# Optimization experiments

Measured on AMD Instinct MI355X. Metric: run time of the kernel, lower is better.

## Reference

```python
import jax, jax.numpy as jnp
import numpy as np

NUM_ENTITIES = 100000
NUM_RELATIONS = 500
EMB_DIM = 256
B = 128
N_CAND = 10000


def setup_inputs() -> dict:
    key = jax.random.key(0)
    k1, k2, k3, k4, k5 = jax.random.split(key, 5)
    # xavier_uniform bound for an (N, D) embedding matrix: sqrt(6/(N+D))
    be = float(np.sqrt(6.0 / (NUM_ENTITIES + EMB_DIM)))
    br = float(np.sqrt(6.0 / (NUM_RELATIONS + EMB_DIM)))
    entity_emb = jax.random.uniform(k1, (NUM_ENTITIES, EMB_DIM), jnp.float32, -be, be)
    relation_emb = jax.random.uniform(k2, (NUM_RELATIONS, EMB_DIM), jnp.float32, -br, br)
    heads = jax.random.randint(k3, (B,), 0, NUM_ENTITIES)
    relations = jax.random.randint(k4, (B,), 0, NUM_RELATIONS)
    tails = jax.random.randint(k5, (N_CAND,), 0, NUM_ENTITIES)
    return {
        "entity_emb": entity_emb,
        "relation_emb": relation_emb,
        "heads": heads,
        "relations": relations,
        "tails": tails,
    }


def reference(entity_emb, relation_emb, heads, relations, tails):
    # score_mode='multi_tails', p=2, dropout=0 (eval)
    h = entity_emb[heads]          # [B, D]
    r = relation_emb[relations]    # [B, D]
    t = entity_emb[tails]          # [N_cand, D]
    left = h + r                   # [B, D]
    # elementwise broadcast L2 distance (donot_use_mm_for_euclid_dist)
    diff = left[:, None, :] - t[None, :, :]          # [B, N_cand, D]
    out = -jnp.sqrt(jnp.sum(diff * diff, axis=-1))   # [B, N_cand]
    return out
```

## Files before the change

### kernel.cpp

```cpp
#include <hip/hip_runtime.h>
#include <math.h>


#define NUM_HEADS 128
#define NCAND     10000
#define EDIM      256
#define BM        64
#define BN        64
#define BK        16

__global__ __launch_bounds__(256) void transe_score_kernel(
    const float* __restrict__ entity,
    const float* __restrict__ relation,
    const int*   __restrict__ heads,
    const int*   __restrict__ relations,
    const int*   __restrict__ tails,
    float*       __restrict__ out)
{
    __shared__ float As[BK][BM];
    __shared__ float Bs[BK][BN];

    const int tid = threadIdx.x;
    const int n0  = blockIdx.x * BN;
    const int m0  = blockIdx.y * BM;

    const int srow = tid & 63;
    const int skq  = tid >> 6;

    const int am = m0 + srow;
    const float* __restrict__ pah = entity   + (size_t)heads[am]     * EDIM;
    const float* __restrict__ par = relation + (size_t)relations[am] * EDIM;

    int bn = n0 + srow;
    if (bn > NCAND - 1) bn = NCAND - 1;
    const float* __restrict__ pb = entity + (size_t)tails[bn] * EDIM;

    const int tx = tid & 15;
    const int ty = tid >> 4;

    float acc[4][4] = {};

    for (int k0 = 0; k0 < EDIM; k0 += BK) {
        float4 vh = *reinterpret_cast<const float4*>(pah + k0 + skq * 4);
        float4 vr = *reinterpret_cast<const float4*>(par + k0 + skq * 4);
        As[skq * 4 + 0][srow] = vh.x + vr.x;
        As[skq * 4 + 1][srow] = vh.y + vr.y;
        As[skq * 4 + 2][srow] = vh.z + vr.z;
        As[skq * 4 + 3][srow] = vh.w + vr.w;
        float4 vb = *reinterpret_cast<const float4*>(pb + k0 + skq * 4);
        Bs[skq * 4 + 0][srow] = vb.x;
        Bs[skq * 4 + 1][srow] = vb.y;
        Bs[skq * 4 + 2][srow] = vb.z;
        Bs[skq * 4 + 3][srow] = vb.w;
        __syncthreads();

        #pragma unroll
        for (int kk = 0; kk < BK; ++kk) {
            float4 a4 = *reinterpret_cast<const float4*>(&As[kk][ty * 4]);
            float4 b4 = *reinterpret_cast<const float4*>(&Bs[kk][tx * 4]);
            float a[4] = {a4.x, a4.y, a4.z, a4.w};
            float b[4] = {b4.x, b4.y, b4.z, b4.w};
            #pragma unroll
            for (int i = 0; i < 4; ++i)
                #pragma unroll
                for (int j = 0; j < 4; ++j) {
                    float d = a[i] - b[j];
                    acc[i][j] = fmaf(d, d, acc[i][j]);
                }
        }
        __syncthreads();
    }

    const int n = n0 + tx * 4;
    if (n < NCAND) {
        #pragma unroll
        for (int i = 0; i < 4; ++i) {
            const int m = m0 + ty * 4 + i;
            float4 o;
            o.x = -sqrtf(acc[i][0]);
            o.y = -sqrtf(acc[i][1]);
            o.z = -sqrtf(acc[i][2]);
            o.w = -sqrtf(acc[i][3]);
            *reinterpret_cast<float4*>(out + (size_t)m * NCAND + n) = o;
        }
    }
}

extern "C" void kernel_launch(void* const* d_in, const int* in_sizes, int n_in,
                              void* d_out, int out_size, void* d_ws, size_t ws_size,
                              hipStream_t stream) {
    const float* entity    = (const float*)d_in[0];
    const float* relation  = (const float*)d_in[1];
    const int*   heads     = (const int*)d_in[2];
    const int*   relations = (const int*)d_in[3];
    const int*   tails     = (const int*)d_in[4];
    float*       out       = (float*)d_out;

    const int n_tiles = (NCAND + BN - 1) / BN;
    const int m_tiles = NUM_HEADS / BM;
    dim3 grid(n_tiles, m_tiles);
    dim3 block(256);
    transe_score_kernel<<<grid, block, 0, stream>>>(entity, relation, heads,
                                                    relations, tails, out);
}
```

Measured before the change: 162.2 us.

## Expand L2 distance into norms plus dot product with transposed prep and async LDS loads

Adds a prep kernel that gathers tail and head+relation rows into transposed, padded workspace buffers and computes partial squared norms. The main kernel then runs a plain FMA GEMM using the identity |a-b|^2 = |a|^2 + |b|^2 - 2ab, with double-buffered global_load_lds staging and BK raised to 32. This removes the subtract from the inner loop and makes the tile loads coalesced. In exchange it adds a second launch, extra workspace traffic, and floating-point cancellation error from the expanded form, clamped at zero.

```diff
diff --git a/kernel.cpp b/kernel.cpp
--- a/kernel.cpp
+++ b/kernel.cpp
@@ -2,85 +2,157 @@
 #include <math.h>
 
 
-#define NUM_HEADS 128
-#define NCAND     10000
-#define EDIM      256
-#define BM        64
-#define BN        64
-#define BK        16
+#define NHEADS   128
+#define NCAND    10000
+#define NPAD     10048
+#define EDIM     256
+#define BM       64
+#define BN       64
+#define BK       32
+#define KSTEPS   (EDIM / BK)
 
-__global__ __launch_bounds__(256) void transe_score_kernel(
-    const float* __restrict__ entity,
-    const float* __restrict__ relation,
-    const int*   __restrict__ heads,
-    const int*   __restrict__ relations,
-    const int*   __restrict__ tails,
-    float*       __restrict__ out)
+#define TT_OFF   0
+#define LT_OFF   (EDIM * NPAD)
+#define TP_OFF   (LT_OFF + EDIM * NHEADS)
+#define LP_OFF   (TP_OFF + 4 * NPAD)
+
+#define GLL(gsrc, ldst) \
+  __builtin_amdgcn_global_load_lds( \
+      (const __attribute__((address_space(1))) void*)(gsrc), \
+      (__attribute__((address_space(3))) void*)(ldst), 16, 0, 0)
+
+__global__ __launch_bounds__(256) void transe_prep(
+    const float* __restrict__ entity, const float* __restrict__ relation,
+    const int* __restrict__ heads, const int* __restrict__ relations,
+    const int* __restrict__ tails, float* __restrict__ ws)
 {
-    __shared__ float As[BK][BM];
-    __shared__ float Bs[BK][BN];
+    float* __restrict__ TT = ws + TT_OFF;
+    float* __restrict__ LT = ws + LT_OFF;
+    float* __restrict__ TP = ws + TP_OFF;
+    float* __restrict__ LP = ws + LP_OFF;
+
+    const int tid  = threadIdx.x;
+    const int lane = tid & 63;
+    const int kc   = tid >> 6;
+    const int b    = blockIdx.x;
+
+    if (b < 157) {
+        const int n = b * 64 + lane;
+        if (n >= NCAND) return;
+        const float* __restrict__ row = entity + (size_t)tails[n] * EDIM;
+        float p = 0.f;
+        #pragma unroll
+        for (int i = 0; i < 16; ++i) {
+            const int k = kc * 64 + i * 4;
+            float4 v = *reinterpret_cast<const float4*>(row + k);
+            TT[(size_t)(k + 0) * NPAD + n] = v.x;
+            TT[(size_t)(k + 1) * NPAD + n] = v.y;
+            TT[(size_t)(k + 2) * NPAD + n] = v.z;
+            TT[(size_t)(k + 3) * NPAD + n] = v.w;
+            p = fmaf(v.x, v.x, p); p = fmaf(v.y, v.y, p);
+            p = fmaf(v.z, v.z, p); p = fmaf(v.w, v.w, p);
+        }
+        TP[kc * NPAD + n] = p;
+    } else {
+        const int m = (b - 157) * 64 + lane;
+        const float* __restrict__ eh = entity   + (size_t)heads[m]     * EDIM;
+        const float* __restrict__ rr = relation + (size_t)relations[m] * EDIM;
+        float p = 0.f;
+        #pragma unroll
+        for (int i = 0; i < 16; ++i) {
+            const int k = kc * 64 + i * 4;
+            float4 a = *reinterpret_cast<const float4*>(eh + k);
+            float4 c = *reinterpret_cast<const float4*>(rr + k);
+            float4 s;
+            s.x = a.x + c.x; s.y = a.y + c.y; s.z = a.z + c.z; s.w = a.w + c.w;
+            LT[(k + 0) * NHEADS + m] = s.x;
+            LT[(k + 1) * NHEADS + m] = s.y;
+            LT[(k + 2) * NHEADS + m] = s.z;
+            LT[(k + 3) * NHEADS + m] = s.w;
+            p = fmaf(s.x, s.x, p); p = fmaf(s.y, s.y, p);
+            p = fmaf(s.z, s.z, p); p = fmaf(s.w, s.w, p);
+        }
+        LP[kc * NHEADS + m] = p;
+    }
+}
+
+__global__ __launch_bounds__(256) void transe_gemm(
+    const float* __restrict__ ws, float* __restrict__ out)
+{
+    const float* __restrict__ TT = ws + TT_OFF;
+    const float* __restrict__ LT = ws + LT_OFF;
+    const float* __restrict__ TP = ws + TP_OFF;
+    const float* __restrict__ LP = ws + LP_OFF;
+
+    __shared__ float As[2][BK][BM];
+    __shared__ float Bs[2][BK][BN];
 
     const int tid = threadIdx.x;
+    const int w   = tid >> 6;
+    const int l   = tid & 63;
+    const int kr  = l >> 4;
+    const int cq  = (l & 15) * 4;
     const int n0  = blockIdx.x * BN;
     const int m0  = blockIdx.y * BM;
-
-    const int srow = tid & 63;
-    const int skq  = tid >> 6;
-
-    const int am = m0 + srow;
-    const float* __restrict__ pah = entity   + (size_t)heads[am]     * EDIM;
-    const float* __restrict__ par = relation + (size_t)relations[am] * EDIM;
-
-    int bn = n0 + srow;
-    if (bn > NCAND - 1) bn = NCAND - 1;
-    const float* __restrict__ pb = entity + (size_t)tails[bn] * EDIM;
-
-    const int tx = tid & 15;
-    const int ty = tid >> 4;
+    const int tx  = tid & 15;
+    const int ty  = tid >> 4;
 
     float acc[4][4] = {};
 
-    for (int k0 = 0; k0 < EDIM; k0 += BK) {
-        float4 vh = *reinterpret_cast<const float4*>(pah + k0 + skq * 4);
-        float4 vr = *reinterpret_cast<const float4*>(par + k0 + skq * 4);
-        As[skq * 4 + 0][srow] = vh.x + vr.x;
-        As[skq * 4 + 1][srow] = vh.y + vr.y;
-        As[skq * 4 + 2][srow] = vh.z + vr.z;
-        As[skq * 4 + 3][srow] = vh.w + vr.w;
-        float4 vb = *reinterpret_cast<const float4*>(pb + k0 + skq * 4);
-        Bs[skq * 4 + 0][srow] = vb.x;
-        Bs[skq * 4 + 1][srow] = vb.y;
-        Bs[skq * 4 + 2][srow] = vb.z;
-        Bs[skq * 4 + 3][srow] = vb.w;
-        __syncthreads();
+    #define STAGE(step, buf)                                                    \
+        {                                                                       \
+            const int k0_ = (step) * BK;                                        \
+            _Pragma("unroll")                                                   \
+            for (int j = 0; j < 2; ++j) {                                       \
+                const int kl = 4 * w + 16 * j;                                  \
+                const float* sA = LT + (size_t)(k0_ + kl + kr) * NHEADS + m0 + cq; \
+                const float* sB = TT + (size_t)(k0_ + kl + kr) * NPAD   + n0 + cq; \
+                GLL(sA, &As[buf][kl][0]);                                       \
+                GLL(sB, &Bs[buf][kl][0]);                                       \
+            }                                                                   \
+        }
 
+    STAGE(0, 0);
+    asm volatile("s_waitcnt vmcnt(0)" ::: "memory");
+    __builtin_amdgcn_s_barrier();
+
+    for (int t = 0; t < KSTEPS; ++t) {
+        const int buf = t & 1;
+        if (t < KSTEPS - 1) STAGE(t + 1, buf ^ 1);
         #pragma unroll
         for (int kk = 0; kk < BK; ++kk) {
-            float4 a4 = *reinterpret_cast<const float4*>(&As[kk][ty * 4]);
-            float4 b4 = *reinterpret_cast<const float4*>(&Bs[kk][tx * 4]);
+            float4 a4 = *reinterpret_cast<const float4*>(&As[buf][kk][ty * 4]);
+            float4 b4 = *reinterpret_cast<const float4*>(&Bs[buf][kk][tx * 4]);
             float a[4] = {a4.x, a4.y, a4.z, a4.w};
             float b[4] = {b4.x, b4.y, b4.z, b4.w};
             #pragma unroll
             for (int i = 0; i < 4; ++i)
                 #pragma unroll
-                for (int j = 0; j < 4; ++j) {
-                    float d = a[i] - b[j];
-                    acc[i][j] = fmaf(d, d, acc[i][j]);
-                }
+                for (int jj = 0; jj < 4; ++jj)
+                    acc[i][jj] = fmaf(a[i], b[jj], acc[i][jj]);
         }
-        __syncthreads();
+        asm volatile("s_waitcnt vmcnt(0)" ::: "memory");
+        __builtin_amdgcn_s_barrier();
     }
 
     const int n = n0 + tx * 4;
+    float4 tn = {0.f, 0.f, 0.f, 0.f};
+    #pragma unroll
+    for (int c = 0; c < 4; ++c) {
+        float4 v = *reinterpret_cast<const float4*>(TP + c * NPAD + n);
+        tn.x += v.x; tn.y += v.y; tn.z += v.z; tn.w += v.w;
+    }
     if (n < NCAND) {
         #pragma unroll
         for (int i = 0; i < 4; ++i) {
             const int m = m0 + ty * 4 + i;
+            const float ln = LP[0 * NHEADS + m] + LP[1 * NHEADS + m] +
+                             LP[2 * NHEADS + m] + LP[3 * NHEADS + m];
             float4 o;
-            o.x = -sqrtf(acc[i][0]);
-            o.y = -sqrtf(acc[i][1]);
-            o.z = -sqrtf(acc[i][2]);
-            o.w = -sqrtf(acc[i][3]);
+            o.x = -sqrtf(fmaxf(ln + tn.x - 2.f * acc[i][0], 0.f));
+            o.y = -sqrtf(fmaxf(ln + tn.y - 2.f * acc[i][1], 0.f));
+            o.z = -sqrtf(fmaxf(ln + tn.z - 2.f * acc[i][2], 0.f));
+            o.w = -sqrtf(fmaxf(ln + tn.w - 2.f * acc[i][3], 0.f));
             *reinterpret_cast<float4*>(out + (size_t)m * NCAND + n) = o;
         }
     }
@@ -94,12 +166,10 @@
     const int*   heads     = (const int*)d_in[2];
     const int*   relations = (const int*)d_in[3];
     const int*   tails     = (const int*)d_in[4];
+    float*       ws        = (float*)d_ws;
     float*       out       = (float*)d_out;
 
-    const int n_tiles = (NCAND + BN - 1) / BN;
-    const int m_tiles = NUM_HEADS / BM;
-    dim3 grid(n_tiles, m_tiles);
-    dim3 block(256);
-    transe_score_kernel<<<grid, block, 0, stream>>>(entity, relation, heads,
-                                                    relations, tails, out);
+    transe_prep<<<dim3(159), dim3(256), 0, stream>>>(entity, relation, heads,
+                                                     relations, tails, ws);
+    transe_gemm<<<dim3(157, 2), dim3(256), 0, stream>>>(ws, out);
 }
```

After: 160.6 us. No clear change (-1.0%).

## Rewrite L2 distance as norm expansion using split-bf16 MFMA GEMM

Applied to the files above, without the earlier changes.

Replaces the direct elementwise squared-difference loop with the expansion ||a||²+||b||²−2a·b. A prep kernel gathers the rows, forms h+r, computes row norms, and splits each fp32 value into bf16 hi and lo parts. A second kernel computes the dot products with bf16 MFMA using three hi/lo products, and stages tiles through global_load_lds double buffering. This moves the work onto matrix cores, at the cost of an extra launch, workspace traffic, and the cancellation error of the norm expansion.

```diff
diff --git a/kernel.cpp b/kernel.cpp
--- a/kernel.cpp
+++ b/kernel.cpp
@@ -2,86 +2,183 @@
 #include <math.h>
 
 
-#define NUM_HEADS 128
-#define NCAND     10000
-#define EDIM      256
-#define BM        64
-#define BN        64
-#define BK        16
-
-__global__ __launch_bounds__(256) void transe_score_kernel(
-    const float* __restrict__ entity,
-    const float* __restrict__ relation,
-    const int*   __restrict__ heads,
-    const int*   __restrict__ relations,
-    const int*   __restrict__ tails,
-    float*       __restrict__ out)
+#define NHEADS 128
+#define NCAND  10000
+#define NPAD   10048
+#define EDIM   256
+#define BM     64
+#define BN     64
+#define BK     32
+#define KSTEPS (EDIM / BK)
+
+#define THI_B  0
+#define TLO_B  (NPAD * EDIM * 2)
+#define LHI_B  (TLO_B + NPAD * EDIM * 2)
+#define LLO_B  (LHI_B + NHEADS * EDIM * 2)
+#define TP_B   (LLO_B + NHEADS * EDIM * 2)
+#define LP_B   (TP_B + NPAD * 4)
+
+typedef __attribute__((ext_vector_type(8))) short bf16x8;
+typedef __attribute__((ext_vector_type(4))) float f32x4;
+
+__device__ inline unsigned short bf16_rn(float x, float& back) {
+    unsigned int u = __float_as_uint(x);
+    unsigned int r = (u + 0x7FFFu + ((u >> 16) & 1u)) >> 16;
+    back = __uint_as_float(r << 16);
+    return (unsigned short)r;
+}
+
+__global__ __launch_bounds__(256) void transe_prep(
+    const float* __restrict__ entity, const float* __restrict__ relation,
+    const int* __restrict__ heads, const int* __restrict__ relations,
+    const int* __restrict__ tails, char* __restrict__ ws)
 {
-    __shared__ float As[BK][BM];
-    __shared__ float Bs[BK][BN];
+    short* __restrict__ Thi = (short*)(ws + THI_B);
+    short* __restrict__ Tlo = (short*)(ws + TLO_B);
+    short* __restrict__ Lhi = (short*)(ws + LHI_B);
+    short* __restrict__ Llo = (short*)(ws + LLO_B);
+    float* __restrict__ TP  = (float*)(ws + TP_B);
+    float* __restrict__ LP  = (float*)(ws + LP_B);
+
+    __shared__ float pn[64][4];
+
+    const int tid  = threadIdx.x;
+    const int lane = tid & 63;
+    const int kc   = tid >> 6;
+    const int b    = blockIdx.x;
+    const bool isT = (b < 157);
+
+    int row;
+    const float* s0;
+    const float* s1 = nullptr;
+    short *dhi, *dlo;
+    float* dp;
+    if (isT) {
+        row = b * 64 + lane;
+        const int n = row > NCAND - 1 ? NCAND - 1 : row;
+        s0  = entity + (size_t)tails[n] * EDIM;
+        dhi = Thi + (size_t)row * EDIM;
+        dlo = Tlo + (size_t)row * EDIM;
+        dp  = TP + row;
+    } else {
+        row = (b - 157) * 64 + lane;
+        s0  = entity   + (size_t)heads[row]     * EDIM;
+        s1  = relation + (size_t)relations[row] * EDIM;
+        dhi = Lhi + (size_t)row * EDIM;
+        dlo = Llo + (size_t)row * EDIM;
+        dp  = LP + row;
+    }
+
+    float p = 0.f;
+    #pragma unroll
+    for (int q = 0; q < 8; ++q) {
+        const int k0 = kc * 64 + q * 8;
+        float4 xa = *(const float4*)(s0 + k0);
+        float4 xb = *(const float4*)(s0 + k0 + 4);
+        float x[8] = {xa.x, xa.y, xa.z, xa.w, xb.x, xb.y, xb.z, xb.w};
+        if (!isT) {
+            float4 ya = *(const float4*)(s1 + k0);
+            float4 yb = *(const float4*)(s1 + k0 + 4);
+            x[0] += ya.x; x[1] += ya.y; x[2] += ya.z; x[3] += ya.w;
+            x[4] += yb.x; x[5] += yb.y; x[6] += yb.z; x[7] += yb.w;
+        }
+        bf16x8 vhi, vlo;
+        #pragma unroll
+        for (int j = 0; j < 8; ++j) {
+            float back;
+            vhi[j] = (short)bf16_rn(x[j], back);
+            float lo = x[j] - back;
+            float lb;
+            vlo[j] = (short)bf16_rn(lo, lb);
+            p = fmaf(x[j], x[j], p);
+        }
+        *(bf16x8*)(dhi + k0) = vhi;
+        *(bf16x8*)(dlo + k0) = vlo;
+    }
+    pn[lane][kc] = p;
+    __syncthreads();
+    if (kc == 0)
+        *dp = pn[lane][0] + pn[lane][1] + pn[lane][2] + pn[lane][3];
+}
+
+#define GLL(g, l_) __builtin_amdgcn_global_load_lds( \
+    (const __attribute__((address_space(1))) void*)(g), \
+    (__attribute__((address_space(3))) void*)(l_), 16, 0, 0)
+
+__global__ __launch_bounds__(256) void transe_gemm(
+    const char* __restrict__ ws, float* __restrict__ out)
+{
+    const short* __restrict__ Thi = (const short*)(ws + THI_B);
+    const short* __restrict__ Tlo = (const short*)(ws + TLO_B);
+    const short* __restrict__ Lhi = (const short*)(ws + LHI_B);
+    const short* __restrict__ Llo = (const short*)(ws + LLO_B);
+    const float* __restrict__ TP  = (const float*)(ws + TP_B);
+    const float* __restrict__ LP  = (const float*)(ws + LP_B);
+
+    __shared__ short smem[2][4][BM * BK];
 
     const int tid = threadIdx.x;
+    const int w   = tid >> 6;
+    const int l   = tid & 63;
     const int n0  = blockIdx.x * BN;
     const int m0  = blockIdx.y * BM;
 
-    const int srow = tid & 63;
-    const int skq  = tid >> 6;
-
-    const int am = m0 + srow;
-    const float* __restrict__ pah = entity   + (size_t)heads[am]     * EDIM;
-    const float* __restrict__ par = relation + (size_t)relations[am] * EDIM;
-
-    int bn = n0 + srow;
-    if (bn > NCAND - 1) bn = NCAND - 1;
-    const float* __restrict__ pb = entity + (size_t)tails[bn] * EDIM;
-
-    const int tx = tid & 15;
-    const int ty = tid >> 4;
-
-    float acc[4][4] = {};
-
-    for (int k0 = 0; k0 < EDIM; k0 += BK) {
-        float4 vh = *reinterpret_cast<const float4*>(pah + k0 + skq * 4);
-        float4 vr = *reinterpret_cast<const float4*>(par + k0 + skq * 4);
-        As[skq * 4 + 0][srow] = vh.x + vr.x;
-        As[skq * 4 + 1][srow] = vh.y + vr.y;
-        As[skq * 4 + 2][srow] = vh.z + vr.z;
-        As[skq * 4 + 3][srow] = vh.w + vr.w;
-        float4 vb = *reinterpret_cast<const float4*>(pb + k0 + skq * 4);
-        Bs[skq * 4 + 0][srow] = vb.x;
-        Bs[skq * 4 + 1][srow] = vb.y;
-        Bs[skq * 4 + 2][srow] = vb.z;
-        Bs[skq * 4 + 3][srow] = vb.w;
-        __syncthreads();
-
+    const short* gbase;
+    int rbase;
+    if      (w == 0) { gbase = Lhi; rbase = m0; }
+    else if (w == 1) { gbase = Llo; rbase = m0; }
+    else if (w == 2) { gbase = Thi; rbase = n0; }
+    else             { gbase = Tlo; rbase = n0; }
+    const short* gl = gbase + (size_t)(rbase + (l >> 2)) * EDIM + (l & 3) * 8;
+    short* ld0 = &smem[0][w][0];
+
+    #define STAGE(t, buf)                                                   \
+        {                                                                   \
+            _Pragma("unroll")                                               \
+            for (int j = 0; j < 4; ++j)                                     \
+                GLL(gl + (size_t)(16 * j) * EDIM + (t) * BK,                \
+                    ld0 + (buf) * 8192 + j * 512);                          \
+        }
+
+    f32x4 acc[4] = {};
+
+    STAGE(0, 0);
+    asm volatile("s_waitcnt vmcnt(0)" ::: "memory");
+    __builtin_amdgcn_s_barrier();
+
+    for (int t = 0; t < KSTEPS; ++t) {
+        const int buf = t & 1;
+        if (t < KSTEPS - 1) STAGE(t + 1, buf ^ 1);
+
+        const int fo = (l & 15) * BK + (l >> 4) * 8;
+        bf16x8 ahi = *(const bf16x8*)(&smem[buf][0][16 * w * BK + fo]);
+        bf16x8 alo = *(const bf16x8*)(&smem[buf][1][16 * w * BK + fo]);
         #pragma unroll
-        for (int kk = 0; kk < BK; ++kk) {
-            float4 a4 = *reinterpret_cast<const float4*>(&As[kk][ty * 4]);
-            float4 b4 = *reinterpret_cast<const float4*>(&Bs[kk][tx * 4]);
-            float a[4] = {a4.x, a4.y, a4.z, a4.w};
-            float b[4] = {b4.x, b4.y, b4.z, b4.w};
+        for (int nf = 0; nf < 4; ++nf) {
+            bf16x8 bhi = *(const bf16x8*)(&smem[buf][2][16 * nf * BK + fo]);
+            bf16x8 blo = *(const bf16x8*)(&smem[buf][3][16 * nf * BK + fo]);
+            acc[nf] = __builtin_amdgcn_mfma_f32_16x16x32_bf16(ahi, bhi, acc[nf], 0, 0, 0);
+            acc[nf] = __builtin_amdgcn_mfma_f32_16x16x32_bf16(ahi, blo, acc[nf], 0, 0, 0);
+            acc[nf] = __builtin_amdgcn_mfma_f32_16x16x32_bf16(alo, bhi, acc[nf], 0, 0, 0);
+        }
+
+        asm volatile("s_waitcnt vmcnt(0)" ::: "memory");
+        __builtin_amdgcn_s_barrier();
+    }
+
+    const int cb = l & 15;
+    const int rq = l >> 4;
+    #pragma unroll
+    for (int nf = 0; nf < 4; ++nf) {
+        const int col = n0 + 16 * nf + cb;
+        if (col < NCAND) {
+            const float tn = TP[col];
             #pragma unroll
-            for (int i = 0; i < 4; ++i)
-                #pragma unroll
-                for (int j = 0; j < 4; ++j) {
-                    float d = a[i] - b[j];
-                    acc[i][j] = fmaf(d, d, acc[i][j]);
-                }
-        }
-        __syncthreads();
-    }
-
-    const int n = n0 + tx * 4;
-    if (n < NCAND) {
-        #pragma unroll
-        for (int i = 0; i < 4; ++i) {
-            const int m = m0 + ty * 4 + i;
-            float4 o;
-            o.x = -sqrtf(acc[i][0]);
-            o.y = -sqrtf(acc[i][1]);
-            o.z = -sqrtf(acc[i][2]);
-            o.w = -sqrtf(acc[i][3]);
-            *reinterpret_cast<float4*>(out + (size_t)m * NCAND + n) = o;
+            for (int r = 0; r < 4; ++r) {
+                const int rowm = m0 + 16 * w + rq * 4 + r;
+                const float v  = LP[rowm] + tn - 2.f * acc[nf][r];
+                out[(size_t)rowm * NCAND + col] = -sqrtf(fmaxf(v, 0.f));
+            }
         }
     }
 }
@@ -94,12 +191,10 @@
     const int*   heads     = (const int*)d_in[2];
     const int*   relations = (const int*)d_in[3];
     const int*   tails     = (const int*)d_in[4];
+    char*        ws        = (char*)d_ws;
     float*       out       = (float*)d_out;
 
-    const int n_tiles = (NCAND + BN - 1) / BN;
-    const int m_tiles = NUM_HEADS / BM;
-    dim3 grid(n_tiles, m_tiles);
-    dim3 block(256);
-    transe_score_kernel<<<grid, block, 0, stream>>>(entity, relation, heads,
-                                                    relations, tails, out);
-}
+    transe_prep<<<dim3(159), dim3(256), 0, stream>>>(entity, relation, heads,
+                                                     relations, tails, ws);
+    transe_gemm<<<dim3(157, 2), dim3(256), 0, stream>>>(ws, out);
+}
```

New measurement: 153.1 us. 5.6% less time.

## Compute L2 distances via norm expansion with split-bf16 MFMA

Applied to the files above, without the earlier changes.

Replaces the scalar fp32 broadcast-difference loop with the expansion ||a||^2 + ||b||^2 - 2ab. The dot products run on bf16 MFMA using a hi/lo split (three products) to approximate fp32 accuracy. All 128 heads now go in one block tile, so each tail row is read only once, and global loads are double-buffered through LDS. The expansion can cancel catastrophically for close vectors (clamped at zero), and the split-bf16 approximation may lose precision compared with the exact difference form.

```diff
diff --git a/kernel.cpp b/kernel.cpp
--- a/kernel.cpp
+++ b/kernel.cpp
@@ -2,86 +2,157 @@
 #include <math.h>
 
 
-#define NUM_HEADS 128
-#define NCAND     10000
-#define EDIM      256
-#define BM        64
-#define BN        64
-#define BK        16
+#define NHEADS 128
+#define NCAND  10000
+#define EDIM   256
+#define BM     128
+#define BN     64
+#define BK     32
+#define KSTEPS (EDIM / BK)
 
-__global__ __launch_bounds__(256) void transe_score_kernel(
-    const float* __restrict__ entity,
-    const float* __restrict__ relation,
-    const int*   __restrict__ heads,
-    const int*   __restrict__ relations,
-    const int*   __restrict__ tails,
-    float*       __restrict__ out)
+typedef __attribute__((ext_vector_type(8))) short bf16x8;
+typedef __attribute__((ext_vector_type(4))) float f32x4;
+
+__device__ inline unsigned short bf16hi(float x) {
+    unsigned int u = __float_as_uint(x);
+    return (unsigned short)((u + 0x7FFFu + ((u >> 16) & 1u)) >> 16);
+}
+
+__global__ __launch_bounds__(256, 1) void transe_fused(
+    const float* __restrict__ entity, const float* __restrict__ relation,
+    const int* __restrict__ heads, const int* __restrict__ relations,
+    const int* __restrict__ tails, float* __restrict__ out)
 {
-    __shared__ float As[BK][BM];
-    __shared__ float Bs[BK][BN];
+    __shared__ short sm[2][12288];
+    __shared__ float LPs[BM];
+    __shared__ float TNs[BN];
 
     const int tid = threadIdx.x;
+    const int w   = tid >> 6;
+    const int l   = tid & 63;
     const int n0  = blockIdx.x * BN;
-    const int m0  = blockIdx.y * BM;
 
-    const int srow = tid & 63;
-    const int skq  = tid >> 6;
+    const int arow = tid >> 2;
+    const int kco  = (tid & 3) * 8;
+    const int soff = (tid >> 6) * 512 + ((tid >> 2) & 15) * 32 + (tid & 3) * 8;
 
-    const int am = m0 + srow;
-    const float* __restrict__ pah = entity   + (size_t)heads[am]     * EDIM;
-    const float* __restrict__ par = relation + (size_t)relations[am] * EDIM;
+    const float* __restrict__ ph0 = entity   + (size_t)heads[arow]           * EDIM + kco;
+    const float* __restrict__ pr0 = relation + (size_t)relations[arow]       * EDIM + kco;
+    const float* __restrict__ ph1 = entity   + (size_t)heads[arow + 64]      * EDIM + kco;
+    const float* __restrict__ pr1 = relation + (size_t)relations[arow + 64]  * EDIM + kco;
+    int bn = n0 + arow; if (bn > NCAND - 1) bn = NCAND - 1;
+    const float* __restrict__ pt  = entity + (size_t)tails[bn] * EDIM + kco;
 
-    int bn = n0 + srow;
-    if (bn > NCAND - 1) bn = NCAND - 1;
-    const float* __restrict__ pb = entity + (size_t)tails[bn] * EDIM;
+    float xa0[8], xa1[8], xb[8];
+    float an0 = 0.f, an1 = 0.f, bnm = 0.f;
+    f32x4 acc[2][4] = {};
 
-    const int tx = tid & 15;
-    const int ty = tid >> 4;
+    auto load_tile = [&](int s) {
+        const int k0 = s * BK;
+        #pragma unroll
+        for (int c = 0; c < 2; ++c) {
+            float4 h0 = *(const float4*)(ph0 + k0 + 4 * c);
+            float4 r0 = *(const float4*)(pr0 + k0 + 4 * c);
+            float4 h1 = *(const float4*)(ph1 + k0 + 4 * c);
+            float4 r1 = *(const float4*)(pr1 + k0 + 4 * c);
+            float4 bv = *(const float4*)(pt  + k0 + 4 * c);
+            xa0[4*c+0] = h0.x + r0.x; xa0[4*c+1] = h0.y + r0.y;
+            xa0[4*c+2] = h0.z + r0.z; xa0[4*c+3] = h0.w + r0.w;
+            xa1[4*c+0] = h1.x + r1.x; xa1[4*c+1] = h1.y + r1.y;
+            xa1[4*c+2] = h1.z + r1.z; xa1[4*c+3] = h1.w + r1.w;
+            xb[4*c+0]  = bv.x; xb[4*c+1] = bv.y; xb[4*c+2] = bv.z; xb[4*c+3] = bv.w;
+        }
+    };
 
-    float acc[4][4] = {};
+    auto convert_write = [&](int buf) {
+        short* base = &sm[buf][0];
+        bf16x8 h0, l0, h1, l1, hb, lb;
+        #pragma unroll
+        for (int j = 0; j < 8; ++j) {
+            float x = xa0[j];
+            an0 = fmaf(x, x, an0);
+            unsigned short hh = bf16hi(x);
+            h0[j] = (short)hh;
+            l0[j] = (short)bf16hi(x - __uint_as_float((unsigned)hh << 16));
+            x = xa1[j];
+            an1 = fmaf(x, x, an1);
+            hh = bf16hi(x);
+            h1[j] = (short)hh;
+            l1[j] = (short)bf16hi(x - __uint_as_float((unsigned)hh << 16));
+            x = xb[j];
+            bnm = fmaf(x, x, bnm);
+            hh = bf16hi(x);
+            hb[j] = (short)hh;
+            lb[j] = (short)bf16hi(x - __uint_as_float((unsigned)hh << 16));
+        }
+        *(bf16x8*)(base + soff)               = h0;
+        *(bf16x8*)(base + 2048 + soff)        = h1;
+        *(bf16x8*)(base + 4096 + soff)        = l0;
+        *(bf16x8*)(base + 4096 + 2048 + soff) = l1;
+        *(bf16x8*)(base + 8192 + soff)        = hb;
+        *(bf16x8*)(base + 10240 + soff)       = lb;
+    };
 
-    for (int k0 = 0; k0 < EDIM; k0 += BK) {
-        float4 vh = *reinterpret_cast<const float4*>(pah + k0 + skq * 4);
-        float4 vr = *reinterpret_cast<const float4*>(par + k0 + skq * 4);
-        As[skq * 4 + 0][srow] = vh.x + vr.x;
-        As[skq * 4 + 1][srow] = vh.y + vr.y;
-        As[skq * 4 + 2][srow] = vh.z + vr.z;
-        As[skq * 4 + 3][srow] = vh.w + vr.w;
-        float4 vb = *reinterpret_cast<const float4*>(pb + k0 + skq * 4);
-        Bs[skq * 4 + 0][srow] = vb.x;
-        Bs[skq * 4 + 1][srow] = vb.y;
-        Bs[skq * 4 + 2][srow] = vb.z;
-        Bs[skq * 4 + 3][srow] = vb.w;
-        __syncthreads();
+    auto compute = [&](int buf) {
+        const short* base = &sm[buf][0];
+        const int fo = (l & 15) * 32 + (l >> 4) * 8;
+        bf16x8 ah[2], al[2];
+        #pragma unroll
+        for (int mf = 0; mf < 2; ++mf) {
+            ah[mf] = *(const bf16x8*)(base + (2 * w + mf) * 512 + fo);
+            al[mf] = *(const bf16x8*)(base + 4096 + (2 * w + mf) * 512 + fo);
+        }
+        #pragma unroll
+        for (int nf = 0; nf < 4; ++nf) {
+            bf16x8 bh = *(const bf16x8*)(base + 8192  + nf * 512 + fo);
+            bf16x8 bl = *(const bf16x8*)(base + 10240 + nf * 512 + fo);
+            #pragma unroll
+            for (int mf = 0; mf < 2; ++mf) {
+                acc[mf][nf] = __builtin_amdgcn_mfma_f32_16x16x32_bf16(ah[mf], bh, acc[mf][nf], 0, 0, 0);
+                acc[mf][nf] = __builtin_amdgcn_mfma_f32_16x16x32_bf16(ah[mf], bl, acc[mf][nf], 0, 0, 0);
+                acc[mf][nf] = __builtin_amdgcn_mfma_f32_16x16x32_bf16(al[mf], bh, acc[mf][nf], 0, 0, 0);
+            }
+        }
+    };
 
-        #pragma unroll
-        for (int kk = 0; kk < BK; ++kk) {
-            float4 a4 = *reinterpret_cast<const float4*>(&As[kk][ty * 4]);
-            float4 b4 = *reinterpret_cast<const float4*>(&Bs[kk][tx * 4]);
-            float a[4] = {a4.x, a4.y, a4.z, a4.w};
-            float b[4] = {b4.x, b4.y, b4.z, b4.w};
-            #pragma unroll
-            for (int i = 0; i < 4; ++i)
-                #pragma unroll
-                for (int j = 0; j < 4; ++j) {
-                    float d = a[i] - b[j];
-                    acc[i][j] = fmaf(d, d, acc[i][j]);
-                }
-        }
+    load_tile(0);
+    convert_write(0);
+    __syncthreads();
+    #pragma unroll
+    for (int t = 0; t < KSTEPS; ++t) {
+        const int buf = t & 1;
+        if (t < KSTEPS - 1) load_tile(t + 1);
+        compute(buf);
+        if (t < KSTEPS - 1) convert_write(buf ^ 1);
         __syncthreads();
     }
 
-    const int n = n0 + tx * 4;
-    if (n < NCAND) {
-        #pragma unroll
-        for (int i = 0; i < 4; ++i) {
-            const int m = m0 + ty * 4 + i;
-            float4 o;
-            o.x = -sqrtf(acc[i][0]);
-            o.y = -sqrtf(acc[i][1]);
-            o.z = -sqrtf(acc[i][2]);
-            o.w = -sqrtf(acc[i][3]);
-            *reinterpret_cast<float4*>(out + (size_t)m * NCAND + n) = o;
+    an0 += __shfl_xor(an0, 1); an0 += __shfl_xor(an0, 2);
+    an1 += __shfl_xor(an1, 1); an1 += __shfl_xor(an1, 2);
+    bnm += __shfl_xor(bnm, 1); bnm += __shfl_xor(bnm, 2);
+    if ((tid & 3) == 0) {
+        LPs[arow]      = an0;
+        LPs[arow + 64] = an1;
+        TNs[arow]      = bnm;
+    }
+    __syncthreads();
+
+    const int cb = l & 15;
+    const int rq = l >> 4;
+    #pragma unroll
+    for (int nf = 0; nf < 4; ++nf) {
+        const int col = n0 + 16 * nf + cb;
+        if (col < NCAND) {
+            const float tn = TNs[16 * nf + cb];
+            #pragma unroll
+            for (int mf = 0; mf < 2; ++mf) {
+                #pragma unroll
+                for (int r = 0; r < 4; ++r) {
+                    const int m = 32 * w + 16 * mf + rq * 4 + r;
+                    const float v = LPs[m] + tn - 2.f * acc[mf][nf][r];
+                    out[(size_t)m * NCAND + col] = -sqrtf(fmaxf(v, 0.f));
+                }
+            }
         }
     }
 }
@@ -96,10 +167,6 @@
     const int*   tails     = (const int*)d_in[4];
     float*       out       = (float*)d_out;
 
-    const int n_tiles = (NCAND + BN - 1) / BN;
-    const int m_tiles = NUM_HEADS / BM;
-    dim3 grid(n_tiles, m_tiles);
-    dim3 block(256);
-    transe_score_kernel<<<grid, block, 0, stream>>>(entity, relation, heads,
-                                                    relations, tails, out);
+    transe_fused<<<dim3((NCAND + BN - 1) / BN), dim3(256), 0, stream>>>(
+        entity, relation, heads, relations, tails, out);
 }
```

After: 149.8 us. -7.6%, faster.
